# Optimization experiments

Hardware: AMD Instinct MI355X
Metric: run time of the kernel (lower is better)

## Reference

```python
import jax, jax.numpy as jnp
import numpy as np

N = 100000  # nodes
E = 1600000  # edges
D_IN = 64
D_H = 64


def _sage_conv(x, src, dst, w_l, b_l, w_r):
    """PyG SAGEConv (mean aggr): lin_l(mean_j x_j) + lin_r(x_i).
    w_l, w_r: [out, in]; b_l: [out]."""
    # scatter-mean of source features onto target nodes
    msg_sum = jax.ops.segment_sum(x[src], dst, num_segments=N)  # [N, in]
    cnt = jax.ops.segment_sum(jnp.ones((src.shape[0],), x.dtype), dst, num_segments=N)
    mean = msg_sum / jnp.maximum(cnt, 1.0)[:, None]
    return mean @ w_l.T + b_l + x @ w_r.T


def setup_inputs() -> dict:
    key = jax.random.key(0)
    ks = jax.random.split(key, 8)
    x = jax.random.normal(ks[0], (N, D_IN), dtype=jnp.float32)
    edge_index = jax.random.randint(ks[1], (2, E), 0, N, dtype=jnp.int64)
    s = 1.0 / np.sqrt(D_IN)
    w_l1 = jax.random.uniform(ks[2], (D_H, D_IN), jnp.float32, -s, s)
    b_l1 = jnp.zeros((D_H,), jnp.float32)
    w_r1 = jax.random.uniform(ks[3], (D_H, D_IN), jnp.float32, -s, s)
    s2 = 1.0 / np.sqrt(D_H)
    w_l2 = jax.random.uniform(ks[4], (D_H, D_H), jnp.float32, -s2, s2)
    b_l2 = jnp.zeros((D_H,), jnp.float32)
    w_r2 = jax.random.uniform(ks[5], (D_H, D_H), jnp.float32, -s2, s2)
    return {"x": x, "edge_index": edge_index,
            "w_l1": w_l1, "b_l1": b_l1, "w_r1": w_r1,
            "w_l2": w_l2, "b_l2": b_l2, "w_r2": w_r2}


def reference(x, edge_index, w_l1, b_l1, w_r1, w_l2, b_l2, w_r2):
    src, dst = edge_index[0], edge_index[1]
    h = jax.nn.relu(_sage_conv(x, src, dst, w_l1, b_l1, w_r1))
    out = _sage_conv(h, src, dst, w_l2, b_l2, w_r2)
    return out
```

## Files before the change

kernel.cpp:

```cpp
#include <hip/hip_runtime.h>

#define N_NODES 100000
#define N_EDGES 1600000
#define D 64

#define BSHIFT 7
#define BNODES (1 << BSHIFT)
#define NB ((N_NODES + BNODES - 1) / BNODES)
#define PB 256
#define TILE ((N_EDGES + PB - 1) / PB)
#define CAP 2432
#define MAXB 4096
#define CAST_BLKS 512
#define QBLKS ((N_NODES * D / 4 + 1023) / 1024)
#define HPARTS (N_NODES / 16)

typedef __attribute__((ext_vector_type(8))) short short8;
typedef __attribute__((ext_vector_type(4))) float float4v;
typedef __attribute__((ext_vector_type(2))) unsigned uint2v;
typedef __attribute__((ext_vector_type(4))) unsigned uint4v;

__device__ __forceinline__ unsigned short f2bf(float f) {
    unsigned u = __float_as_uint(f);
    u = (u + 0x7fffu + ((u >> 16) & 1u)) >> 16;
    return (unsigned short)u;
}
__device__ __forceinline__ unsigned cvtpk(float a, float b) {
    unsigned r;
    asm("v_cvt_pk_bf16_f32 %0, %1, %2" : "=v"(r) : "v"(a), "v"(b));
    return r;
}

__device__ __forceinline__ float4 bf16x4_to_f4(uint2 v) {
    float4 r;
    r.x = __uint_as_float(v.x << 16);
    r.y = __uint_as_float(v.x & 0xffff0000u);
    r.z = __uint_as_float(v.y << 16);
    r.w = __uint_as_float(v.y & 0xffff0000u);
    return r;
}

__global__ __launch_bounds__(1024) void front(const float* __restrict__ x,
                                              unsigned short* __restrict__ xb,
                                              float* __restrict__ partial,
                                              const int* __restrict__ src,
                                              const int* __restrict__ dst,
                                              int* __restrict__ gcnt,
                                              int* __restrict__ part) {
    __shared__ float red[16];
    __shared__ int hist[NB];
    __shared__ int lcur[NB];
    __shared__ int gbase[NB];
    __shared__ int ebuf[TILE];
    __shared__ int gtgt[TILE];

    int tid = threadIdx.x;

    if (blockIdx.x < CAST_BLKS) {
        float m = 0.0f;
        int stride = CAST_BLKS * 1024;
        for (int i = blockIdx.x * 1024 + tid; i < N_NODES * D / 4; i += stride) {
            float4 v = ((const float4*)x)[i];
            ushort4 o;
            o.x = f2bf(v.x); o.y = f2bf(v.y); o.z = f2bf(v.z); o.w = f2bf(v.w);
            ((ushort4*)xb)[i] = o;
            m = fmaxf(m, fmaxf(fmaxf(fabsf(v.x), fabsf(v.y)), fmaxf(fabsf(v.z), fabsf(v.w))));
        }
        for (int off = 32; off >= 1; off >>= 1) m = fmaxf(m, __shfl_xor(m, off, 64));
        if ((tid & 63) == 0) red[tid >> 6] = m;
        __syncthreads();
        if (tid == 0) {
            float mm = 0.0f;
#pragma unroll
            for (int w = 0; w < 16; ++w) mm = fmaxf(mm, red[w]);
            partial[blockIdx.x] = mm;
        }
        return;
    }

    int bid = blockIdx.x - CAST_BLKS;
    for (int i = tid; i < NB; i += 1024) hist[i] = 0;
    __syncthreads();

    int lo = bid * TILE;

    unsigned pk[7];
    int bk[7];
#pragma unroll
    for (int k = 0; k < 7; ++k) {
        int e = lo + tid + k * 1024;
        if (tid + k * 1024 < TILE) {
            int dd = dst[e];
            int ss = src[e];
            int b = dd >> BSHIFT;
            pk[k] = ((unsigned)ss << BSHIFT) | (unsigned)(dd & (BNODES - 1));
            bk[k] = b;
            atomicAdd(&hist[b], 1);
        } else {
            bk[k] = -1;
        }
    }
    __syncthreads();

    int h = (tid < NB) ? hist[tid] : 0;
    if (tid < NB)
        gbase[tid] = tid * CAP + (h ? atomicAdd(&gcnt[tid], h) : 0);
    int val = h;
    gtgt[tid] = val;
    __syncthreads();
    for (int off = 1; off < 1024; off <<= 1) {
        int u = (tid >= off) ? gtgt[tid - off] : 0;
        __syncthreads();
        val += u;
        gtgt[tid] = val;
        __syncthreads();
    }
    if (tid < NB) {
        hist[tid] = val - h;
        lcur[tid] = val - h;
    }
    __syncthreads();

#pragma unroll
    for (int k = 0; k < 7; ++k) {
        if (bk[k] >= 0) {
            int b = bk[k];
            int p = atomicAdd(&lcur[b], 1);
            ebuf[p] = (int)pk[k];
            gtgt[p] = gbase[b] + (p - hist[b]);
        }
    }
    __syncthreads();

    for (int i = tid; i < TILE; i += 1024)
        part[gtgt[i]] = ebuf[i];
}

__device__ __forceinline__ void quant_body(int i, const unsigned short* __restrict__ inb,
                                           unsigned char* __restrict__ out8, float s) {
    uint2 v = ((const uint2*)inb)[i];
    float4 f = bf16x4_to_f4(v);
    int q0 = min(127, max(-127, __float2int_rn(f.x * s))) + 128;
    int q1 = min(127, max(-127, __float2int_rn(f.y * s))) + 128;
    int q2 = min(127, max(-127, __float2int_rn(f.z * s))) + 128;
    int q3 = min(127, max(-127, __float2int_rn(f.w * s))) + 128;
    ((unsigned*)out8)[i] = (unsigned)q0 | ((unsigned)q1 << 8) |
                           ((unsigned)q2 << 16) | ((unsigned)q3 << 24);
}

__device__ __forceinline__ float fold_partials(const float* __restrict__ partial,
                                               int n, float* red, float* bc) {
    int tid = threadIdx.x;
    float m = 0.0f;
    for (int i = tid; i < n; i += 1024) m = fmaxf(m, partial[i]);
    for (int off = 32; off >= 1; off >>= 1) m = fmaxf(m, __shfl_xor(m, off, 64));
    if ((tid & 63) == 0) red[tid >> 6] = m;
    __syncthreads();
    if (tid == 0) {
        float mm = 0.0f;
#pragma unroll
        for (int w = 0; w < 16; ++w) mm = fmaxf(mm, red[w]);
        *bc = mm;
    }
    __syncthreads();
    return *bc;
}

__global__ __launch_bounds__(1024) void back(const int* __restrict__ gcnt,
                                             const int* __restrict__ part,
                                             int* __restrict__ row_ptr,
                                             int* __restrict__ sorted_src,
                                             const unsigned short* __restrict__ xb,
                                             unsigned char* __restrict__ x8,
                                             const float* __restrict__ partial,
                                             unsigned* __restrict__ amax_store,
                                             const float* __restrict__ wl1,
                                             const float* __restrict__ wr1,
                                             unsigned short* __restrict__ wb1,
                                             const float* __restrict__ wl2,
                                             const float* __restrict__ wr2,
                                             unsigned short* __restrict__ wb2) {
    __shared__ int in_buf[MAXB];
    __shared__ int out_buf[MAXB];
    __shared__ int hist[BNODES];
    __shared__ int exs[BNODES];
    __shared__ int cursor[BNODES];
    __shared__ float red[16];
    __shared__ float bc;

    int tid = threadIdx.x;

    if (blockIdx.x >= NB + QBLKS) {
        int i = (blockIdx.x - NB - QBLKS) * 1024 + tid;
        int j = i & 8191;
        int o = j >> 7, kk = j & 127;
        if (i < 8192) {
            float v = (kk < D) ? wl1[o * D + kk] : wr1[o * D + (kk - D)];
            wb1[j] = f2bf(v);
        } else {
            float v = (kk < D) ? wl2[o * D + kk] : wr2[o * D + (kk - D)];
            wb2[j] = f2bf(v);
        }
        return;
    }

    if (blockIdx.x >= NB) {
        float A = fold_partials(partial, CAST_BLKS, red, &bc);
        if (blockIdx.x == NB && tid == 0) *amax_store = __float_as_uint(A);
        float s = (A > 0.0f) ? 127.0f / A : 0.0f;
        int i = (blockIdx.x - NB) * 1024 + tid;
        if (i < N_NODES * D / 4) quant_body(i, xb, x8, s);
        return;
    }

    int k = blockIdx.x;

    int v = (tid < NB) ? gcnt[tid] : 0;
    int val = v;
    in_buf[tid] = val;
    __syncthreads();
    for (int off = 1; off < 1024; off <<= 1) {
        int u = (tid >= off) ? in_buf[tid - off] : 0;
        __syncthreads();
        val += u;
        in_buf[tid] = val;
        __syncthreads();
    }
    int base  = (k > 0) ? in_buf[k - 1] : 0;
    int count = gcnt[k];
    int src0  = k * CAP;
    __syncthreads();

    for (int i = tid; i < BNODES; i += 1024) hist[i] = 0;
    __syncthreads();

    for (int i = tid; i < count; i += 1024) {
        int w = part[src0 + i];
        in_buf[i] = w;
        atomicAdd(&hist[w & (BNODES - 1)], 1);
    }
    __syncthreads();
    if (tid < 64) {
        int a = hist[2 * tid], b = hist[2 * tid + 1];
        int s = a + b, incl = s;
        for (int off = 1; off < 64; off <<= 1) {
            int t = __shfl_up(incl, off, 64);
            if (tid >= off) incl += t;
        }
        int excl = incl - s;
        exs[2 * tid] = excl;
        exs[2 * tid + 1] = excl + a;
    }
    __syncthreads();
    if (tid < BNODES) {
        int node = k * BNODES + tid;
        if (node < N_NODES) row_ptr[node] = base + exs[tid];
        cursor[tid] = exs[tid];
    }
    if (tid == 0 && k == NB - 1) row_ptr[N_NODES] = N_EDGES;
    __syncthreads();
    for (int i = tid; i < count; i += 1024) {
        int w = in_buf[i];
        int r = atomicAdd(&cursor[w & (BNODES - 1)], 1);
        out_buf[r] = w >> BSHIFT;
    }
    __syncthreads();
    for (int i = tid; i < count; i += 1024)
        sorted_src[base + i] = out_buf[i];
}

__global__ __launch_bounds__(1024) void quant8f(const unsigned short* __restrict__ inb,
                                                unsigned char* __restrict__ out8,
                                                const float* __restrict__ partial,
                                                unsigned* __restrict__ amax_store) {
    __shared__ float red[16];
    __shared__ float bc;
    float A = fold_partials(partial, HPARTS, red, &bc);
    if (blockIdx.x == 0 && threadIdx.x == 0) *amax_store = __float_as_uint(A);
    float s = (A > 0.0f) ? 127.0f / A : 0.0f;
    int i = blockIdx.x * 1024 + threadIdx.x;
    if (i < N_NODES * D / 4) quant_body(i, inb, out8, s);
}

#define ACCW(w, kk) { aLo[kk] += (w) & 0x00FF00FFu; \
                      aHi[kk] += __builtin_amdgcn_perm(0u, (w), 0x04030401u); }
#define ACC4(v) { ACCW((v).x, 0) ACCW((v).y, 1) ACCW((v).z, 2) ACCW((v).w, 3) }

__global__ __launch_bounds__(512, 8) void sage8(
    const int* __restrict__ row_ptr, const int* __restrict__ nbr,
    const unsigned char* __restrict__ tab8,
    const unsigned short* __restrict__ selfb,
    const unsigned* __restrict__ amax_bits,
    const unsigned short* __restrict__ wb,
    const float* __restrict__ b_l,
    float* __restrict__ out,
    unsigned short* __restrict__ outb,
    float* __restrict__ hpart,
    int apply_relu)
{
    __shared__ unsigned short a_s[16][136];
    __shared__ float st[16][68];
    __shared__ float bias[D];
    __shared__ float wred[4];

    int tid = threadIdx.x;
    if (tid < D) bias[tid] = b_l[tid];

    int wave = tid >> 6;
    int lane = tid & 63;
    int nsel = lane >> 5;
    int l32  = lane & 31;
    int g    = l32 >> 2;
    int c    = l32 & 3;
    int arow = wave * 2 + nsel;
    int node = blockIdx.x * 16 + arow;

    float A  = __uint_as_float(*amax_bits);
    float gs = A * (1.0f / 127.0f);

    int begin = row_ptr[node];
    int end   = row_ptr[node + 1];

    uint2v xv = {0, 0};
    if (l32 < 16)
        xv = __builtin_nontemporal_load((const uint2v*)&selfb[(size_t)node * D + 4 * l32]);

    unsigned c16 = (unsigned)(c << 4);
    unsigned aLo[4] = {0, 0, 0, 0};
    unsigned aHi[4] = {0, 0, 0, 0};
    for (int base = begin; base < end; base += 32) {
        int m = end - base; if (m > 32) m = 32;
        int id = (l32 < m) ? __builtin_nontemporal_load(&nbr[base + l32]) : 0;
        int s0 = __shfl(id, nsel * 32 + g,      64);
        int s1 = __shfl(id, nsel * 32 + 8 + g,  64);
        int s2 = __shfl(id, nsel * 32 + 16 + g, 64);
        int s3 = __shfl(id, nsel * 32 + 24 + g, 64);
        bool a0 = (g < m), a1 = (8 + g < m), a2 = (16 + g < m), a3 = (24 + g < m);
        uint4 v0, v1, v2, v3;
        if (a0) v0 = *(const uint4*)(tab8 + ((((unsigned)s0) << 6) | c16));
        if (a1) v1 = *(const uint4*)(tab8 + ((((unsigned)s1) << 6) | c16));
        if (a2) v2 = *(const uint4*)(tab8 + ((((unsigned)s2) << 6) | c16));
        if (a3) v3 = *(const uint4*)(tab8 + ((((unsigned)s3) << 6) | c16));
        if (a0) { ACC4(v0) }
        if (a1) { ACC4(v1) }
        if (a2) { ACC4(v2) }
        if (a3) { ACC4(v3) }
    }

#pragma unroll
    for (int off = 4; off <= 16; off <<= 1) {
#pragma unroll
        for (int k = 0; k < 4; ++k) {
            aLo[k] += (unsigned)__shfl_xor((int)aLo[k], off, 64);
            aHi[k] += (unsigned)__shfl_xor((int)aHi[k], off, 64);
        }
    }

    int   deg  = end - begin;
    float invd = 1.0f / fmaxf((float)deg, 1.0f);
    float sc   = gs * invd;
    float nofs = -128.0f * (float)deg * sc;

    {
        unsigned lo01 = (g & 2) ? aLo[1] : aLo[0];
        unsigned lo23 = (g & 2) ? aLo[3] : aLo[2];
        unsigned wLo  = (g & 4) ? lo23 : lo01;
        unsigned hi01 = (g & 2) ? aHi[1] : aHi[0];
        unsigned hi23 = (g & 2) ? aHi[3] : aHi[2];
        unsigned wHi  = (g & 4) ? hi23 : hi01;
        int sh = (g & 1) << 4;
        float d0 = (float)((wLo >> sh) & 0xFFFFu);
        float d1 = (float)((wHi >> sh) & 0xFFFFu);
        float f0 = fmaf(d0, sc, nofs);
        float f1 = fmaf(d1, sc, nofs);
        *(unsigned*)&a_s[arow][16 * c + 2 * g] = cvtpk(f0, f1);
    }
    if (l32 < 16)
        *(uint2v*)&a_s[arow][64 + 4 * l32] = xv;
    __syncthreads();

    if (wave < 4) {
        int quad = lane >> 4;
        int cc   = lane & 15;

        float4v acc = {0.f, 0.f, 0.f, 0.f};
#pragma unroll
        for (int kk = 0; kk < 4; ++kk) {
            short8 af = *(const short8*)&a_s[cc][kk * 32 + quad * 8];
            short8 bf = *(const short8*)(wb + (size_t)(wave * 16 + cc) * 128 + kk * 32 + quad * 8);
            acc = __builtin_amdgcn_mfma_f32_16x16x32_bf16(af, bf, acc, 0, 0, 0);
        }

        int o = wave * 16 + cc;
        float bv = bias[o];
        float vv[4];
#pragma unroll
        for (int r = 0; r < 4; ++r) {
            float v = acc[r] + bv;
            if (apply_relu) v = fmaxf(v, 0.0f);
            vv[r] = v;
            st[quad * 4 + r][o] = v;
        }
        if (hpart) {
            float m = fmaxf(fmaxf(fabsf(vv[0]), fabsf(vv[1])),
                            fmaxf(fabsf(vv[2]), fabsf(vv[3])));
            for (int off = 32; off >= 1; off >>= 1) m = fmaxf(m, __shfl_xor(m, off, 64));
            if (lane == 0) wred[wave] = m;
        }
    }
    __syncthreads();

    if (wave >= 4) {
        int idx = tid - 256;
        if (outb) {
            if (idx < 128) {
                int row = idx >> 3, c8 = idx & 7;
                const float* p = &st[row][c8 * 8];
                float4v f0 = *(const float4v*)p;
                float4v f1 = *(const float4v*)(p + 4);
                uint4v q;
                q[0] = cvtpk(f0[0], f0[1]); q[1] = cvtpk(f0[2], f0[3]);
                q[2] = cvtpk(f1[0], f1[1]); q[3] = cvtpk(f1[2], f1[3]);
                __builtin_nontemporal_store(q,
                    (uint4v*)&outb[((size_t)(blockIdx.x * 16 + row)) * D + 8 * c8]);
            }
        } else {
            int row = idx >> 4, c4 = idx & 15;
            uint4v q = *(const uint4v*)&st[row][c4 * 4];
            __builtin_nontemporal_store(q,
                (uint4v*)&out[((size_t)(blockIdx.x * 16 + row)) * D + 4 * c4]);
        }
        if (hpart && idx == 0)
            hpart[blockIdx.x] = fmaxf(fmaxf(wred[0], wred[1]), fmaxf(wred[2], wred[3]));
    }
}

extern "C" void kernel_launch(void* const* d_in, const int* in_sizes, int n_in,
                              void* d_out, int out_size, void* d_ws, size_t ws_size,
                              hipStream_t stream) {
    const float* x    = (const float*)d_in[0];
    const int*   ei   = (const int*)d_in[1];
    const float* w_l1 = (const float*)d_in[2];
    const float* b_l1 = (const float*)d_in[3];
    const float* w_r1 = (const float*)d_in[4];
    const float* w_l2 = (const float*)d_in[5];
    const float* b_l2 = (const float*)d_in[6];
    const float* w_r2 = (const float*)d_in[7];
    float* out = (float*)d_out;

    const int* src = ei;
    const int* dst = ei + N_EDGES;

    unsigned* scales   = (unsigned*)d_ws;
    int* gcnt          = (int*)d_ws + 4;
    int* row_ptr       = gcnt + NB;
    int* part          = row_ptr + 100004;
    int* sorted_src    = part + NB * CAP;
    unsigned short* xb = (unsigned short*)(sorted_src + N_EDGES);
    unsigned short* hb = xb + (size_t)N_NODES * D;
    unsigned char* x8  = (unsigned char*)(hb + (size_t)N_NODES * D);
    unsigned char* h8  = x8 + (size_t)N_NODES * D;
    unsigned short* wb1 = (unsigned short*)(h8 + (size_t)N_NODES * D);
    unsigned short* wb2 = wb1 + D * 2 * D;
    float* partA       = (float*)(wb2 + D * 2 * D);

    (void)hipMemsetAsync(d_ws, 0, 16 + NB * sizeof(int), stream);

    front<<<dim3(CAST_BLKS + PB), dim3(1024), 0, stream>>>(x, xb, partA,
                                                           src, dst, gcnt, part);
    back<<<dim3(NB + QBLKS + 16), dim3(1024), 0, stream>>>(gcnt, part,
                                                           row_ptr, sorted_src,
                                                           xb, x8, partA, &scales[0],
                                                           w_l1, w_r1, wb1,
                                                           w_l2, w_r2, wb2);

    dim3 lblk(512);
    dim3 lgrid(N_NODES / 16);
    sage8<<<lgrid, lblk, 0, stream>>>(row_ptr, sorted_src, x8, xb,
                                      &scales[0], wb1, b_l1,
                                      (float*)nullptr, hb, partA, 1);
    quant8f<<<dim3(QBLKS), dim3(1024), 0, stream>>>(hb, h8, partA, &scales[1]);
    sage8<<<lgrid, lblk, 0, stream>>>(row_ptr, sorted_src, h8, hb,
                                      &scales[1], wb2, b_l2,
                                      out, (unsigned short*)nullptr,
                                      (float*)nullptr, 0);
}
```

Measured before the change: 210.3 us.

## Replace global CSR prefix scan with padded per-bucket begin/end arrays

Drops the 1024-wide block-level prefix scan over bucket counts in the sort kernel by placing each bucket's edges at a fixed k*CAP offset, storing separate begin and end arrays per node instead of a contiguous row_ptr. The aggregation kernel reads begin/end directly and loads neighbor ids per lane straight from memory instead of a coalesced load plus four shuffles. This removes many barriers per sort block and some shuffle work, at the cost of a sparser neighbor array, an extra index array read, and more scattered neighbor-id loads.

```diff
diff --git a/kernel.cpp b/kernel.cpp
--- a/kernel.cpp
+++ b/kernel.cpp
@@ -7,6 +7,7 @@
 #define BSHIFT 7
 #define BNODES (1 << BSHIFT)
 #define NB ((N_NODES + BNODES - 1) / BNODES)
+#define NPAD (NB * BNODES)
 #define PB 256
 #define TILE ((N_EDGES + PB - 1) / PB)
 #define CAP 2432
@@ -168,7 +169,8 @@
 
 __global__ __launch_bounds__(1024) void back(const int* __restrict__ gcnt,
                                              const int* __restrict__ part,
-                                             int* __restrict__ row_ptr,
+                                             int* __restrict__ rbeg,
+                                             int* __restrict__ rend,
                                              int* __restrict__ sorted_src,
                                              const unsigned short* __restrict__ xb,
                                              unsigned char* __restrict__ x8,
@@ -214,28 +216,14 @@
     }
 
     int k = blockIdx.x;
-
-    int v = (tid < NB) ? gcnt[tid] : 0;
-    int val = v;
-    in_buf[tid] = val;
-    __syncthreads();
-    for (int off = 1; off < 1024; off <<= 1) {
-        int u = (tid >= off) ? in_buf[tid - off] : 0;
-        __syncthreads();
-        val += u;
-        in_buf[tid] = val;
-        __syncthreads();
-    }
-    int base  = (k > 0) ? in_buf[k - 1] : 0;
+    int base  = k * CAP;
     int count = gcnt[k];
-    int src0  = k * CAP;
-    __syncthreads();
 
     for (int i = tid; i < BNODES; i += 1024) hist[i] = 0;
     __syncthreads();
 
     for (int i = tid; i < count; i += 1024) {
-        int w = part[src0 + i];
+        int w = part[base + i];
         in_buf[i] = w;
         atomicAdd(&hist[w & (BNODES - 1)], 1);
     }
@@ -254,10 +242,12 @@
     __syncthreads();
     if (tid < BNODES) {
         int node = k * BNODES + tid;
-        if (node < N_NODES) row_ptr[node] = base + exs[tid];
+        if (node < N_NODES) {
+            rbeg[node] = base + exs[tid];
+            rend[node] = base + exs[tid] + hist[tid];
+        }
         cursor[tid] = exs[tid];
     }
-    if (tid == 0 && k == NB - 1) row_ptr[N_NODES] = N_EDGES;
     __syncthreads();
     for (int i = tid; i < count; i += 1024) {
         int w = in_buf[i];
@@ -287,7 +277,8 @@
 #define ACC4(v) { ACCW((v).x, 0) ACCW((v).y, 1) ACCW((v).z, 2) ACCW((v).w, 3) }
 
 __global__ __launch_bounds__(512, 8) void sage8(
-    const int* __restrict__ row_ptr, const int* __restrict__ nbr,
+    const int* __restrict__ rbeg, const int* __restrict__ rend,
+    const int* __restrict__ nbr,
     const unsigned char* __restrict__ tab8,
     const unsigned short* __restrict__ selfb,
     const unsigned* __restrict__ amax_bits,
@@ -318,8 +309,8 @@
     float A  = __uint_as_float(*amax_bits);
     float gs = A * (1.0f / 127.0f);
 
-    int begin = row_ptr[node];
-    int end   = row_ptr[node + 1];
+    int begin = rbeg[node];
+    int end   = rend[node];
 
     uint2v xv = {0, 0};
     if (l32 < 16)
@@ -329,13 +320,13 @@
     unsigned aLo[4] = {0, 0, 0, 0};
     unsigned aHi[4] = {0, 0, 0, 0};
     for (int base = begin; base < end; base += 32) {
-        int m = end - base; if (m > 32) m = 32;
-        int id = (l32 < m) ? __builtin_nontemporal_load(&nbr[base + l32]) : 0;
-        int s0 = __shfl(id, nsel * 32 + g,      64);
-        int s1 = __shfl(id, nsel * 32 + 8 + g,  64);
-        int s2 = __shfl(id, nsel * 32 + 16 + g, 64);
-        int s3 = __shfl(id, nsel * 32 + 24 + g, 64);
+        int m = end - base;
         bool a0 = (g < m), a1 = (8 + g < m), a2 = (16 + g < m), a3 = (24 + g < m);
+        int s0 = 0, s1 = 0, s2 = 0, s3 = 0;
+        if (a0) s0 = nbr[base + g];
+        if (a1) s1 = nbr[base + 8 + g];
+        if (a2) s2 = nbr[base + 16 + g];
+        if (a3) s3 = nbr[base + 24 + g];
         uint4 v0, v1, v2, v3;
         if (a0) v0 = *(const uint4*)(tab8 + ((((unsigned)s0) << 6) | c16));
         if (a1) v1 = *(const uint4*)(tab8 + ((((unsigned)s1) << 6) | c16));
@@ -453,10 +444,11 @@
 
     unsigned* scales   = (unsigned*)d_ws;
     int* gcnt          = (int*)d_ws + 4;
-    int* row_ptr       = gcnt + NB;
-    int* part          = row_ptr + 100004;
+    int* rbeg          = gcnt + NB;
+    int* rend          = rbeg + NPAD;
+    int* part          = rend + NPAD;
     int* sorted_src    = part + NB * CAP;
-    unsigned short* xb = (unsigned short*)(sorted_src + N_EDGES);
+    unsigned short* xb = (unsigned short*)(sorted_src + NB * CAP);
     unsigned short* hb = xb + (size_t)N_NODES * D;
     unsigned char* x8  = (unsigned char*)(hb + (size_t)N_NODES * D);
     unsigned char* h8  = x8 + (size_t)N_NODES * D;
@@ -469,18 +461,18 @@
     front<<<dim3(CAST_BLKS + PB), dim3(1024), 0, stream>>>(x, xb, partA,
                                                            src, dst, gcnt, part);
     back<<<dim3(NB + QBLKS + 16), dim3(1024), 0, stream>>>(gcnt, part,
-                                                           row_ptr, sorted_src,
+                                                           rbeg, rend, sorted_src,
                                                            xb, x8, partA, &scales[0],
                                                            w_l1, w_r1, wb1,
                                                            w_l2, w_r2, wb2);
 
     dim3 lblk(512);
     dim3 lgrid(N_NODES / 16);
-    sage8<<<lgrid, lblk, 0, stream>>>(row_ptr, sorted_src, x8, xb,
+    sage8<<<lgrid, lblk, 0, stream>>>(rbeg, rend, sorted_src, x8, xb,
                                       &scales[0], wb1, b_l1,
                                       (float*)nullptr, hb, partA, 1);
     quant8f<<<dim3(QBLKS), dim3(1024), 0, stream>>>(hb, h8, partA, &scales[1]);
-    sage8<<<lgrid, lblk, 0, stream>>>(row_ptr, sorted_src, h8, hb,
+    sage8<<<lgrid, lblk, 0, stream>>>(rbeg, rend, sorted_src, h8, hb,
                                       &scales[1], wb2, b_l2,
                                       out, (unsigned short*)nullptr,
                                       (float*)nullptr, 0);
```

Result: slower. 220.3 us (+4.8%).
